# Performance work log

Measured on AMD Instinct MI355X. Metric: run time of the kernel, lower is better.

Reference implementation:

```python
import jax, jax.numpy as jnp
import numpy as np
import math

N_HEAD = 16
D_MODEL = 1024
D_HEAD = 64
GRID = 28


def _alibi_slopes(heads):
    def pow2(n):
        start = 2 ** (-(2 ** (-(math.log2(n) - 3))))
        return [start * (start ** i) for i in range(n)]
    if math.log2(heads).is_integer():
        return pow2(heads)
    c = 2 ** math.floor(math.log2(heads))
    return pow2(c) + pow2(2 * c)[0::2][: heads - c]


def _teeth_bias(heads):
    # bias[i,j] = |i%14 - j%14| + |i//14 - j//14| (loop in get_bias overwrites the -|j-i| init)
    idx = np.arange(GRID)
    row, col = idx // 14, idx % 14
    b = np.abs(col[:, None] - col[None, :]) + np.abs(row[:, None] - row[None, :])  # [28,28]
    slopes = np.asarray(_alibi_slopes(heads), dtype=np.float32)  # [h]
    return jnp.asarray(slopes[:, None, None] * b[None].astype(np.float32))  # [h,28,28]


def _layer_norm(x, gamma, beta, eps=1e-5):
    mu = jnp.mean(x, axis=-1, keepdims=True)
    var = jnp.var(x, axis=-1, keepdims=True)
    return (x - mu) * jax.lax.rsqrt(var + eps) * gamma + beta


def setup_inputs() -> dict:
    key = jax.random.key(0)
    ks = jax.random.split(key, 6)
    s = 0.02
    return {
        "hidden": jax.random.normal(ks[0], (2048, GRID, D_MODEL), dtype=jnp.float32),
        "wq": jax.random.normal(ks[1], (D_MODEL, N_HEAD * D_HEAD), dtype=jnp.float32) * s,
        "wk": jax.random.normal(ks[2], (D_MODEL, N_HEAD * D_HEAD), dtype=jnp.float32) * s,
        "wv": jax.random.normal(ks[3], (D_MODEL, N_HEAD * D_HEAD), dtype=jnp.float32) * s,
        "wo": jax.random.normal(ks[4], (N_HEAD * D_HEAD, D_MODEL), dtype=jnp.float32) * s,
        "gamma": jnp.ones((D_MODEL,), dtype=jnp.float32),
        "beta": jnp.zeros((D_MODEL,), dtype=jnp.float32),
    }


def reference(hidden, wq, wk, wv, wo, gamma, beta):
    b, s, _ = hidden.shape
    # pre_lnorm: hidden is reassigned to LN(hidden); combined == hidden (memory=None)
    h = _layer_norm(hidden, gamma, beta)
    q = (h @ wq).reshape(b, s, N_HEAD, D_HEAD).transpose(0, 2, 1, 3)  # [b,h,s,d]
    k = (h @ wk).reshape(b, s, N_HEAD, D_HEAD).transpose(0, 2, 1, 3)
    v = (h @ wv).reshape(b, s, N_HEAD, D_HEAD).transpose(0, 2, 1, 3)
    # NOTE: original forward never applies atten_scale -> unscaled dots (faithful)
    scores = jnp.einsum("bhid,bhjd->bhij", q, k)
    scores = scores + _teeth_bias(N_HEAD)[None, :, :s, :s]
    attn = jax.nn.softmax(scores, axis=-1)
    ctx = jnp.einsum("bhij,bhjd->bhid", attn, v)
    ctx = ctx.transpose(0, 2, 1, 3).reshape(b, s, N_HEAD * D_HEAD)
    out = ctx @ wo
    return h + out  # pre_lnorm residual uses the normalized hidden
```

## Files before the change

### kernel.cpp

```cpp
#include <hip/hip_runtime.h>
#include <hip/hip_bf16.h>

typedef unsigned short u16;
typedef __attribute__((ext_vector_type(8))) short bf16x8;
typedef __attribute__((ext_vector_type(4))) float f32x4;

#define DEVINL __device__ __forceinline__

DEVINL u16 f2b(float f) {
    __hip_bfloat16 h = __float2bfloat16(f);
    return __builtin_bit_cast(u16, h);
}
DEVINL float b2f(u16 u) {
    unsigned int x = ((unsigned int)u) << 16;
    return __builtin_bit_cast(float, x);
}
DEVINL int iabs(int x) { return x < 0 ? -x : x; }
DEVINL f32x4 MFMA(bf16x8 a, bf16x8 b, f32x4 c) {
    return __builtin_amdgcn_mfma_f32_16x16x32_bf16(a, b, c, 0, 0, 0);
}

#define GL2LDS(g, s)                                                                     \
    __builtin_amdgcn_global_load_lds(                                                    \
        (const __attribute__((address_space(1))) unsigned int*)(g),                      \
        (__attribute__((address_space(3))) unsigned int*)(s), 16, 0, 0)

__global__ __launch_bounds__(256) void wconv_kernel(const float* __restrict__ wq,
                                                    const float* __restrict__ wk,
                                                    const float* __restrict__ wv,
                                                    const float* __restrict__ wo,
                                                    u16* __restrict__ wqkvt,
                                                    u16* __restrict__ wot) {
    __shared__ float tile[32][33];
    int z = blockIdx.z;
    const float* src = (z == 0) ? wq : (z == 1) ? wk : (z == 2) ? wv : wo;
    int n0 = blockIdx.x * 32, k0 = blockIdx.y * 32;
    int r0 = threadIdx.x >> 5, c = threadIdx.x & 31;
#pragma unroll
    for (int i = 0; i < 4; i++) {
        int r = r0 + i * 8;
        tile[r][c] = src[(size_t)(k0 + r) * 1024 + n0 + c];
    }
    __syncthreads();
    u16* dst = (z < 3) ? wqkvt : wot;
#pragma unroll
    for (int i = 0; i < 4; i++) {
        int r = r0 + i * 8;
        int nn = n0 + r;
        size_t drow = (z < 3) ? ((size_t)(nn >> 6) * 192 + (size_t)z * 64 + (nn & 63))
                              : (size_t)nn;
        dst[drow * 1024 + k0 + c] = f2b(tile[c][r]);
    }
}

__global__ __launch_bounds__(256) void ln_kernel(const float* __restrict__ x,
                                                 const float* __restrict__ gamma,
                                                 const float* __restrict__ beta,
                                                 u16* __restrict__ h) {
    int w = threadIdx.x >> 6, l = threadIdx.x & 63;
    size_t row = (size_t)blockIdx.x * 4 + w;
    const float4* xr = (const float4*)(x + row * 1024);
    float4 v[4];
    float s = 0.f, sq = 0.f;
#pragma unroll
    for (int i = 0; i < 4; i++) {
        v[i] = xr[l + i * 64];
        s += v[i].x + v[i].y + v[i].z + v[i].w;
        sq += v[i].x * v[i].x + v[i].y * v[i].y + v[i].z * v[i].z + v[i].w * v[i].w;
    }
#pragma unroll
    for (int off = 1; off < 64; off <<= 1) {
        s += __shfl_xor(s, off);
        sq += __shfl_xor(sq, off);
    }
    float mu = s * (1.f / 1024.f);
    float var = sq * (1.f / 1024.f) - mu * mu;
    float rstd = rsqrtf(var + 1e-5f);
    const float4* g4 = (const float4*)gamma;
    const float4* b4 = (const float4*)beta;
#pragma unroll
    for (int i = 0; i < 4; i++) {
        float4 g = g4[l + i * 64], b = b4[l + i * 64];
        float y0 = (v[i].x - mu) * rstd * g.x + b.x;
        float y1 = (v[i].y - mu) * rstd * g.y + b.y;
        float y2 = (v[i].z - mu) * rstd * g.z + b.z;
        float y3 = (v[i].w - mu) * rstd * g.w + b.w;
        unsigned int lo = (unsigned int)f2b(y0) | ((unsigned int)f2b(y1) << 16);
        unsigned int hi = (unsigned int)f2b(y2) | ((unsigned int)f2b(y3) << 16);
        uint2 pk;
        pk.x = lo;
        pk.y = hi;
        *(uint2*)(h + row * 1024 + (size_t)(l + i * 64) * 4) = pk;
    }
}

__global__ __launch_bounds__(512, 2) void fused_qkv_attn(const u16* __restrict__ h,
                                                         const u16* __restrict__ wqkvt,
                                                         u16* __restrict__ ctx) {
    __shared__ __align__(16) char smem[53248];
    char* sA = smem;
    char* sB = smem + 28672;
    int t = threadIdx.x;

    int nwg = gridDim.x;
    int cpx = nwg >> 3;
    int wg = ((int)blockIdx.x & 7) * cpx + ((int)blockIdx.x >> 3);
    int x = wg >> 9;
    int i0 = wg & 511;
    int bm = i0 >> 1;
    int head = (x << 1) | (i0 & 1);

    int p16 = t * 16;
    int srow = p16 >> 7;
    int scolb = (p16 & 127) ^ ((srow & 7) << 4);
    const char* aB = (const char*)h + ((size_t)bm * 224 + srow) * 2048 + scolb;
    const char* bB = (const char*)wqkvt + ((size_t)head * 192 + srow) * 2048 + scolb;

    int l = t & 63, w = t >> 6, g = l >> 4, lr = l & 15;
    int wm = w >> 2, wn = w & 3;
    int swz = (lr & 7) << 4;

    f32x4 acc[7][3];
#pragma unroll
    for (int m = 0; m < 7; m++)
#pragma unroll
        for (int n = 0; n < 3; n++) acc[m][n] = {0.f, 0.f, 0.f, 0.f};

#pragma unroll 1
    for (int kt = 0; kt < 16; ++kt) {
        int kb = kt * 128;
#pragma unroll
        for (int i = 0; i < 3; i++) GL2LDS(aB + (size_t)i * 131072 + kb, sA + i * 8192 + p16);
        if (t < 256) GL2LDS(aB + (size_t)3 * 131072 + kb, sA + 3 * 8192 + p16);
#pragma unroll
        for (int i = 0; i < 3; i++) GL2LDS(bB + (size_t)i * 131072 + kb, sB + i * 8192 + p16);
        __syncthreads();
#pragma unroll
        for (int ks = 0; ks < 2; ++ks) {
            bf16x8 af[7], bfv[3];
#pragma unroll
            for (int m = 0; m < 7; m++)
                af[m] = *(const bf16x8*)(sA + (wm * 112 + m * 16 + lr) * 128 +
                                         ((ks * 64 + g * 16) ^ swz));
#pragma unroll
            for (int n = 0; n < 3; n++)
                bfv[n] = *(const bf16x8*)(sB + (wn * 48 + n * 16 + lr) * 128 +
                                          ((ks * 64 + g * 16) ^ swz));
#pragma unroll
            for (int m = 0; m < 7; m++)
#pragma unroll
                for (int n = 0; n < 3; n++) acc[m][n] = MFMA(af[m], bfv[n], acc[m][n]);
        }
        __syncthreads();
    }

    u16* qkb = (u16*)smem;
    u16(*vt)[64][40] = (u16(*)[64][40])smem;
    u16(*spw)[40] = (u16(*)[40])(smem + 28672 + w * 1280);

    int sl = w >> 1, ih = w & 1;
    int rb = sl * 28;
    float slope = exp2f(-0.5f * (float)(head + 1));
    int j0 = lr, j1 = 16 + lr;
    int j0m = j0 % 14, j0d = j0 / 14;
    int j1m = j1 % 14, j1d = j1 / 14;

#pragma unroll 1
    for (int hh = 0; hh < 2; ++hh) {
        if (wm == hh) {
#pragma unroll
            for (int m = 0; m < 7; m++)
#pragma unroll
                for (int n = 0; n < 3; n++) {
                    int col = wn * 48 + n * 16 + lr;
                    if (col < 128) {
#pragma unroll
                        for (int r = 0; r < 4; ++r) {
                            int lrow = m * 16 + g * 4 + r;
                            qkb[lrow * 128 + (col ^ ((lrow & 7) << 3))] = f2b(acc[m][n][r]);
                        }
                    }
                }
        }
        __syncthreads();

        f32x4 sc0 = {0.f, 0.f, 0.f, 0.f}, sc1 = {0.f, 0.f, 0.f, 0.f};
#pragma unroll
        for (int c = 0; c < 2; ++c) {
            int u0 = c * 32 + g * 8;
            int arow = rb + ih * 16 + lr;
            int br0 = rb + lr, br1 = rb + 16 + lr;
            bf16x8 aa = *(const bf16x8*)&qkb[arow * 128 + (u0 ^ ((arow & 7) << 3))];
            bf16x8 b0 = *(const bf16x8*)&qkb[br0 * 128 + ((64 + u0) ^ ((br0 & 7) << 3))];
            bf16x8 b1 = *(const bf16x8*)&qkb[br1 * 128 + ((64 + u0) ^ ((br1 & 7) << 3))];
            sc0 = MFMA(aa, b0, sc0);
            sc1 = MFMA(aa, b1, sc1);
        }
#pragma unroll
        for (int r = 0; r < 4; ++r) {
            int i = ih * 16 + g * 4 + r;
            int im = i % 14, id = i / 14;
            float s0 = sc0[r] + slope * (float)(iabs(im - j0m) + iabs(id - j0d));
            float s1 = (j1 < 28)
                           ? sc1[r] + slope * (float)(iabs(im - j1m) + iabs(id - j1d))
                           : -1e30f;
            float mx = fmaxf(s0, s1);
#pragma unroll
            for (int off = 1; off < 16; off <<= 1) mx = fmaxf(mx, __shfl_xor(mx, off));
            float e0 = __expf(s0 - mx), e1 = __expf(s1 - mx);
            float sm = e0 + e1;
#pragma unroll
            for (int off = 1; off < 16; off <<= 1) sm += __shfl_xor(sm, off);
            float inv = 1.f / sm;
            spw[g * 4 + r][lr] = f2b(e0 * inv);
            spw[g * 4 + r][16 + lr] = f2b(e1 * inv);
        }
        __syncthreads();

        if (t < 256) {
            int s2 = t >> 6, d = t & 63;
#pragma unroll
            for (int j = 28; j < 32; ++j) vt[s2][d][j] = 0;
        }
        if (wm == hh) {
#pragma unroll
            for (int m = 0; m < 7; m++)
#pragma unroll
                for (int n = 0; n < 3; n++) {
                    int col = wn * 48 + n * 16 + lr;
                    if (col >= 128) {
#pragma unroll
                        for (int r = 0; r < 4; ++r) {
                            int lrow = m * 16 + g * 4 + r;
                            int d = col - 128;
                            int s2 = lrow / 28;
                            int j = lrow - s2 * 28;
                            vt[s2][d][j] = f2b(acc[m][n][r]);
                        }
                    }
                }
        }
        __syncthreads();

        bf16x8 pa = *(const bf16x8*)&spw[lr][g * 8];
        f32x4 o[4];
#pragma unroll
        for (int d = 0; d < 4; d++) o[d] = {0.f, 0.f, 0.f, 0.f};
#pragma unroll
        for (int dt = 0; dt < 4; ++dt) {
            bf16x8 bv = *(const bf16x8*)&vt[sl][dt * 16 + lr][g * 8];
            o[dt] = MFMA(pa, bv, o[dt]);
        }
#pragma unroll
        for (int dt = 0; dt < 4; ++dt)
#pragma unroll
            for (int r = 0; r < 4; ++r) {
                int i = ih * 16 + g * 4 + r;
                if (i < 28) {
                    size_t grow = (size_t)bm * 224 + (size_t)hh * 112 + sl * 28 + i;
                    ctx[grow * 1024 + head * 64 + dt * 16 + lr] = f2b(o[dt][r]);
                }
            }
        __syncthreads();
    }
}

template <int OUT_BF16, int RESID>
__global__ __launch_bounds__(256, 2) void gemm_bt(const u16* __restrict__ A,
                                                  const u16* __restrict__ Bt,
                                                  void* __restrict__ Cv,
                                                  const u16* __restrict__ resid,
                                                  int lda, int ldc) {
    __shared__ u16 smem[16384];
    int t = threadIdx.x;

    int nwg = gridDim.x;
    int cpx = nwg >> 3;
    int wg = (blockIdx.x & 7) * cpx + (blockIdx.x >> 3);
    const int sgrp = 448 * 8;
    int sn = wg / sgrp;
    int rem = wg - sn * sgrp;
    int bm = rem >> 3;
    int bn = sn * 8 + (rem & 7);

    const char* Ab = (const char*)A;
    const char* Bb = (const char*)Bt;
    size_t aoffg[4], boffg[4];
#pragma unroll
    for (int i = 0; i < 4; i++) {
        int p = t * 16 + i * 4096;
        int row = p >> 7;
        int colb = (p & 127) ^ ((row & 7) << 4);
        aoffg[i] = (size_t)(bm * 128 + row) * (size_t)lda * 2 + colb;
        boffg[i] = (size_t)(bn * 128 + row) * 2048 + colb;
    }
    char* sA = (char*)smem;
    char* sB = sA + 16384;

    int l = t & 63, w = t >> 6;
    int wm = w >> 1, wn = w & 1, g = l >> 4, lr = l & 15;
    int swz = (lr & 7) << 4;

    f32x4 acc[4][4];
#pragma unroll
    for (int m = 0; m < 4; m++)
#pragma unroll
        for (int n = 0; n < 4; n++) acc[m][n] = {0.f, 0.f, 0.f, 0.f};

    for (int kt = 0; kt < 16; ++kt) {
        int kb = kt * 128;
#pragma unroll
        for (int i = 0; i < 4; i++) GL2LDS(Ab + aoffg[i] + kb, sA + i * 4096 + t * 16);
#pragma unroll
        for (int i = 0; i < 4; i++) GL2LDS(Bb + boffg[i] + kb, sB + i * 4096 + t * 16);
        __syncthreads();
#pragma unroll
        for (int ks = 0; ks < 2; ++ks) {
            bf16x8 af[4], bfv[4];
#pragma unroll
            for (int m = 0; m < 4; m++)
                af[m] = *(const bf16x8*)(sA + (wm * 64 + m * 16 + lr) * 128 +
                                         ((ks * 64 + g * 16) ^ swz));
#pragma unroll
            for (int n = 0; n < 4; n++)
                bfv[n] = *(const bf16x8*)(sB + (wn * 64 + n * 16 + lr) * 128 +
                                          ((ks * 64 + g * 16) ^ swz));
#pragma unroll
            for (int m = 0; m < 4; m++)
#pragma unroll
                for (int n = 0; n < 4; n++)
                    acc[m][n] = MFMA(af[m], bfv[n], acc[m][n]);
        }
        __syncthreads();
    }

    size_t row0 = (size_t)bm * 128 + wm * 64;
    int col0 = bn * 128 + wn * 64;
    if (OUT_BF16) {
        u16* C = (u16*)Cv;
#pragma unroll
        for (int m = 0; m < 4; m++)
#pragma unroll
            for (int n = 0; n < 4; n++)
#pragma unroll
                for (int r = 0; r < 4; r++) {
                    size_t rr = row0 + m * 16 + g * 4 + r;
                    int cc = col0 + n * 16 + lr;
                    C[rr * (size_t)ldc + cc] = f2b(acc[m][n][r]);
                }
    } else {
        float* C = (float*)Cv;
#pragma unroll
        for (int m = 0; m < 4; m++)
#pragma unroll
            for (int n = 0; n < 4; n++)
#pragma unroll
                for (int r = 0; r < 4; r++) {
                    size_t rr = row0 + m * 16 + g * 4 + r;
                    int cc = col0 + n * 16 + lr;
                    float o = acc[m][n][r];
                    if (RESID) o += b2f(resid[rr * 1024 + cc]);
                    C[rr * (size_t)ldc + cc] = o;
                }
    }
}

extern "C" void kernel_launch(void* const* d_in, const int* in_sizes, int n_in,
                              void* d_out, int out_size, void* d_ws, size_t ws_size,
                              hipStream_t stream) {
    (void)in_sizes; (void)n_in; (void)out_size; (void)ws_size;
    const float* hidden = (const float*)d_in[0];
    const float* wq = (const float*)d_in[1];
    const float* wk = (const float*)d_in[2];
    const float* wv = (const float*)d_in[3];
    const float* wo = (const float*)d_in[4];
    const float* gamma = (const float*)d_in[5];
    const float* beta = (const float*)d_in[6];
    float* out = (float*)d_out;

    char* ws = (char*)d_ws;
    u16* h = (u16*)ws;
    u16* ctx = (u16*)(ws + 117440512);
    u16* wqkvt = (u16*)(ws + 234881024);
    u16* wot = (u16*)(ws + 234881024 + 6291456);

    wconv_kernel<<<dim3(32, 32, 4), 256, 0, stream>>>(wq, wk, wv, wo, wqkvt, wot);
    ln_kernel<<<14336, 256, 0, stream>>>(hidden, gamma, beta, h);
    fused_qkv_attn<<<4096, 512, 0, stream>>>(h, wqkvt, ctx);
    gemm_bt<0, 1><<<448 * 8, 256, 0, stream>>>(ctx, wot, out, h, 1024, 1024);
}
```

Measured before the change: 776.9 us.

## Shrink fused QKV-attention block to 112 rows with two waves

The fused QKV projection plus attention kernel now uses 128-thread workgroups that each handle 112 rows (4 sequences) for one head, instead of 512-thread workgroups handling 224 rows. Each wave computes a 112x96 tile with more accumulators, and the two-pass loop over row halves, with its extra barriers, is replaced by a single pass. The intent is to cut synchronisation and raise the number of independent workgroups. In exchange the weight tile is reloaded twice as often per row, and the larger per-wave accumulator set (42 tiles) increases register pressure.

```diff
diff --git a/kernel.cpp b/kernel.cpp
--- a/kernel.cpp
+++ b/kernel.cpp
@@ -94,96 +94,92 @@
     }
 }
 
-__global__ __launch_bounds__(512, 2) void fused_qkv_attn(const u16* __restrict__ h,
-                                                         const u16* __restrict__ wqkvt,
-                                                         u16* __restrict__ ctx) {
-    __shared__ __align__(16) char smem[53248];
+__global__ __launch_bounds__(128) void fused_qkv_attn(const u16* __restrict__ h,
+                                                      const u16* __restrict__ wqkvt,
+                                                      u16* __restrict__ ctx) {
+    __shared__ __align__(16) char smem[38912];
     char* sA = smem;
-    char* sB = smem + 28672;
+    char* sB = smem + 14336;
     int t = threadIdx.x;
 
     int nwg = gridDim.x;
     int cpx = nwg >> 3;
     int wg = ((int)blockIdx.x & 7) * cpx + ((int)blockIdx.x >> 3);
-    int x = wg >> 9;
-    int i0 = wg & 511;
+    int x = wg >> 10;
+    int i0 = wg & 1023;
     int bm = i0 >> 1;
     int head = (x << 1) | (i0 & 1);
 
     int p16 = t * 16;
     int srow = p16 >> 7;
     int scolb = (p16 & 127) ^ ((srow & 7) << 4);
-    const char* aB = (const char*)h + ((size_t)bm * 224 + srow) * 2048 + scolb;
+    const char* aB = (const char*)h + ((size_t)bm * 112 + srow) * 2048 + scolb;
     const char* bB = (const char*)wqkvt + ((size_t)head * 192 + srow) * 2048 + scolb;
 
     int l = t & 63, w = t >> 6, g = l >> 4, lr = l & 15;
-    int wm = w >> 2, wn = w & 3;
     int swz = (lr & 7) << 4;
 
-    f32x4 acc[7][3];
+    f32x4 acc[7][6];
 #pragma unroll
     for (int m = 0; m < 7; m++)
 #pragma unroll
-        for (int n = 0; n < 3; n++) acc[m][n] = {0.f, 0.f, 0.f, 0.f};
+        for (int n = 0; n < 6; n++) acc[m][n] = {0.f, 0.f, 0.f, 0.f};
 
 #pragma unroll 1
     for (int kt = 0; kt < 16; ++kt) {
         int kb = kt * 128;
 #pragma unroll
-        for (int i = 0; i < 3; i++) GL2LDS(aB + (size_t)i * 131072 + kb, sA + i * 8192 + p16);
-        if (t < 256) GL2LDS(aB + (size_t)3 * 131072 + kb, sA + 3 * 8192 + p16);
-#pragma unroll
-        for (int i = 0; i < 3; i++) GL2LDS(bB + (size_t)i * 131072 + kb, sB + i * 8192 + p16);
+        for (int i = 0; i < 7; i++) GL2LDS(aB + (size_t)i * 32768 + kb, sA + i * 2048 + p16);
+#pragma unroll
+        for (int i = 0; i < 12; i++) GL2LDS(bB + (size_t)i * 32768 + kb, sB + i * 2048 + p16);
         __syncthreads();
 #pragma unroll
         for (int ks = 0; ks < 2; ++ks) {
-            bf16x8 af[7], bfv[3];
+            bf16x8 af[7], bfv[6];
 #pragma unroll
             for (int m = 0; m < 7; m++)
-                af[m] = *(const bf16x8*)(sA + (wm * 112 + m * 16 + lr) * 128 +
-                                         ((ks * 64 + g * 16) ^ swz));
-#pragma unroll
-            for (int n = 0; n < 3; n++)
-                bfv[n] = *(const bf16x8*)(sB + (wn * 48 + n * 16 + lr) * 128 +
+                af[m] = *(const bf16x8*)(sA + (m * 16 + lr) * 128 + ((ks * 64 + g * 16) ^ swz));
+#pragma unroll
+            for (int n = 0; n < 6; n++)
+                bfv[n] = *(const bf16x8*)(sB + (w * 96 + n * 16 + lr) * 128 +
                                           ((ks * 64 + g * 16) ^ swz));
 #pragma unroll
             for (int m = 0; m < 7; m++)
 #pragma unroll
-                for (int n = 0; n < 3; n++) acc[m][n] = MFMA(af[m], bfv[n], acc[m][n]);
+                for (int n = 0; n < 6; n++) acc[m][n] = MFMA(af[m], bfv[n], acc[m][n]);
         }
         __syncthreads();
     }
 
     u16* qkb = (u16*)smem;
     u16(*vt)[64][40] = (u16(*)[64][40])smem;
-    u16(*spw)[40] = (u16(*)[40])(smem + 28672 + w * 1280);
-
-    int sl = w >> 1, ih = w & 1;
-    int rb = sl * 28;
+    char* spbase = smem + 28672;
+
+#pragma unroll
+    for (int m = 0; m < 7; m++)
+#pragma unroll
+        for (int n = 0; n < 6; n++) {
+            int col = w * 96 + n * 16 + lr;
+            if (col < 128) {
+#pragma unroll
+                for (int r = 0; r < 4; ++r) {
+                    int row = m * 16 + g * 4 + r;
+                    qkb[row * 128 + (col ^ ((row & 7) << 3))] = f2b(acc[m][n][r]);
+                }
+            }
+        }
+    __syncthreads();
+
     float slope = exp2f(-0.5f * (float)(head + 1));
     int j0 = lr, j1 = 16 + lr;
     int j0m = j0 % 14, j0d = j0 / 14;
     int j1m = j1 % 14, j1d = j1 / 14;
 
-#pragma unroll 1
-    for (int hh = 0; hh < 2; ++hh) {
-        if (wm == hh) {
-#pragma unroll
-            for (int m = 0; m < 7; m++)
-#pragma unroll
-                for (int n = 0; n < 3; n++) {
-                    int col = wn * 48 + n * 16 + lr;
-                    if (col < 128) {
-#pragma unroll
-                        for (int r = 0; r < 4; ++r) {
-                            int lrow = m * 16 + g * 4 + r;
-                            qkb[lrow * 128 + (col ^ ((lrow & 7) << 3))] = f2b(acc[m][n][r]);
-                        }
-                    }
-                }
-        }
-        __syncthreads();
-
+#pragma unroll
+    for (int q = 0; q < 4; ++q) {
+        int seq = w * 2 + (q >> 1), ih = q & 1;
+        int rb = seq * 28;
+        u16(*spw)[40] = (u16(*)[40])(spbase + (w * 4 + q) * 1280);
         f32x4 sc0 = {0.f, 0.f, 0.f, 0.f}, sc1 = {0.f, 0.f, 0.f, 0.f};
 #pragma unroll
         for (int c = 0; c < 2; ++c) {
@@ -215,40 +211,45 @@
             spw[g * 4 + r][lr] = f2b(e0 * inv);
             spw[g * 4 + r][16 + lr] = f2b(e1 * inv);
         }
-        __syncthreads();
-
-        if (t < 256) {
-            int s2 = t >> 6, d = t & 63;
-#pragma unroll
-            for (int j = 28; j < 32; ++j) vt[s2][d][j] = 0;
-        }
-        if (wm == hh) {
-#pragma unroll
-            for (int m = 0; m < 7; m++)
-#pragma unroll
-                for (int n = 0; n < 3; n++) {
-                    int col = wn * 48 + n * 16 + lr;
-                    if (col >= 128) {
-#pragma unroll
-                        for (int r = 0; r < 4; ++r) {
-                            int lrow = m * 16 + g * 4 + r;
-                            int d = col - 128;
-                            int s2 = lrow / 28;
-                            int j = lrow - s2 * 28;
-                            vt[s2][d][j] = f2b(acc[m][n][r]);
-                        }
-                    }
-                }
-        }
-        __syncthreads();
-
+    }
+    __syncthreads();
+
+#pragma unroll
+    for (int it = 0; it < 2; ++it) {
+        int idx = t + it * 128;
+        int s2 = idx >> 6, d = idx & 63;
+#pragma unroll
+        for (int j = 28; j < 32; ++j) vt[s2][d][j] = 0;
+    }
+    if (w == 1) {
+#pragma unroll
+        for (int m = 0; m < 7; m++)
+#pragma unroll
+            for (int n = 2; n < 6; n++) {
+                int col = 96 + n * 16 + lr;
+                int d = col - 128;
+#pragma unroll
+                for (int r = 0; r < 4; ++r) {
+                    int row = m * 16 + g * 4 + r;
+                    int s2 = row / 28;
+                    int j = row - s2 * 28;
+                    vt[s2][d][j] = f2b(acc[m][n][r]);
+                }
+            }
+    }
+    __syncthreads();
+
+#pragma unroll
+    for (int q = 0; q < 4; ++q) {
+        int seq = w * 2 + (q >> 1), ih = q & 1;
+        u16(*spw)[40] = (u16(*)[40])(spbase + (w * 4 + q) * 1280);
         bf16x8 pa = *(const bf16x8*)&spw[lr][g * 8];
         f32x4 o[4];
 #pragma unroll
         for (int d = 0; d < 4; d++) o[d] = {0.f, 0.f, 0.f, 0.f};
 #pragma unroll
         for (int dt = 0; dt < 4; ++dt) {
-            bf16x8 bv = *(const bf16x8*)&vt[sl][dt * 16 + lr][g * 8];
+            bf16x8 bv = *(const bf16x8*)&vt[seq][dt * 16 + lr][g * 8];
             o[dt] = MFMA(pa, bv, o[dt]);
         }
 #pragma unroll
@@ -257,11 +258,11 @@
             for (int r = 0; r < 4; ++r) {
                 int i = ih * 16 + g * 4 + r;
                 if (i < 28) {
-                    size_t grow = (size_t)bm * 224 + (size_t)hh * 112 + sl * 28 + i;
-                    ctx[grow * 1024 + head * 64 + dt * 16 + lr] = f2b(o[dt][r]);
+                    size_t off =
+                        ((size_t)(bm * 4 + seq) * 28 + i) * 1024 + head * 64 + dt * 16 + lr;
+                    ctx[off] = f2b(o[dt][r]);
                 }
             }
-        __syncthreads();
     }
 }
 
@@ -386,6 +387,6 @@
 
     wconv_kernel<<<dim3(32, 32, 4), 256, 0, stream>>>(wq, wk, wv, wo, wqkvt, wot);
     ln_kernel<<<14336, 256, 0, stream>>>(hidden, gamma, beta, h);
-    fused_qkv_attn<<<4096, 512, 0, stream>>>(h, wqkvt, ctx);
+    fused_qkv_attn<<<8192, 128, 0, stream>>>(h, wqkvt, ctx);
     gemm_bt<0, 1><<<448 * 8, 256, 0, stream>>>(ctx, wot, out, h, 1024, 1024);
 }
```

Result: slower. 867.2 us (+11.6%).
